# Optimization experiments

Hardware: AMD Instinct MI355X
Metric: run time of the kernel (lower is better)

Reference implementation:

```python
import jax, jax.numpy as jnp
import numpy as np

V, NJ, NB, NP, NK = 6890, 24, 10, 207, 19
PARENTS = [-1,0,0,0,1,2,3,4,5,6,7,8,9,9,9,12,13,14,16,17,18,19,20,21]


def setup_inputs() -> dict:
    key = jax.random.key(0)
    ks = jax.random.split(key, 9)
    N = 2048
    return {
        "beta": jax.random.normal(ks[0], (N, NB), jnp.float32),
        "theta": jax.random.normal(ks[1], (N, NJ, 3), jnp.float32) * 0.2,
        "trans": jax.random.normal(ks[2], (N, 3), jnp.float32),
        "shapedirs": jax.random.normal(ks[3], (V, 3, NB), jnp.float32) * 0.03,
        "v_template": jax.random.normal(ks[4], (V, 3), jnp.float32),
        "J_regressor": jax.random.uniform(ks[5], (NJ, V), jnp.float32) / V,
        "posedirs": jax.random.normal(ks[6], (V, 3, NP), jnp.float32) * 0.01,
        "weights": jax.nn.softmax(jax.random.normal(ks[7], (V, NJ), jnp.float32) * 4.0, axis=-1),
        "joint_regressor": jax.random.uniform(ks[8], (V, NK), jnp.float32) / V,
    }


def rodrigues(r):
    # r: [M,3] axis-angle -> [M,3,3] rotation matrices
    theta = jnp.maximum(jnp.linalg.norm(r, axis=-1, keepdims=True),
                        jnp.finfo(r.dtype).tiny)  # [M,1]
    rh = r / theta
    c = jnp.cos(theta)[:, :, None]  # [M,1,1]
    s = jnp.sin(theta)[:, :, None]
    z = jnp.zeros_like(rh[:, 0])
    K = jnp.stack([z, -rh[:, 2], rh[:, 1],
                   rh[:, 2], z, -rh[:, 0],
                   -rh[:, 1], rh[:, 0], z], axis=1).reshape(-1, 3, 3)
    outer = rh[:, :, None] * rh[:, None, :]
    return c * jnp.eye(3, dtype=r.dtype) + (1.0 - c) * outer + s * K


def reference(beta, theta, trans, shapedirs, v_template, J_regressor, posedirs, weights, joint_regressor):
    N = beta.shape[0]
    dt = beta.dtype
    v_shaped = jnp.einsum('nb,vcb->nvc', beta, shapedirs) + v_template  # [N,V,3]
    J = jnp.einsum('jv,nvc->njc', J_regressor, v_shaped)                # [N,24,3]
    # pose rotations and pose blendshapes
    R = rodrigues(theta.reshape(-1, 3)).reshape(N, NJ, 3, 3)
    lrotmin = (R[:, 1:] - jnp.eye(3, dtype=dt)).reshape(N, NP)
    v_posed = v_shaped + jnp.einsum('np,vcp->nvc', lrotmin, posedirs)
    # kinematic chain: 24 small 4x4 transforms with parent dependencies
    bottom = jnp.broadcast_to(jnp.array([0., 0., 0., 1.], dtype=dt), (N, 1, 4))
    def make_A(Ri, t):  # [N,3,3],[N,3] -> [N,4,4]
        return jnp.concatenate([jnp.concatenate([Ri, t[:, :, None]], axis=2), bottom], axis=1)
    G = [make_A(R[:, 0], J[:, 0])]
    for i in range(1, NJ):
        p = PARENTS[i]
        G.append(G[p] @ make_A(R[:, i], J[:, i] - J[:, p]))
    G = jnp.stack(G, axis=1)  # [N,24,4,4]
    # subtract rest-pose joint contribution
    Jh = jnp.concatenate([J, jnp.zeros((N, NJ, 1), dt)], axis=2)[..., None]  # [N,24,4,1]
    corr = G @ Jh
    G_rel = G - jnp.concatenate([jnp.zeros((N, NJ, 4, 3), dt), corr], axis=3)
    # linear blend skinning
    T = jnp.einsum('njab,vj->nvab', G_rel, weights)  # [N,V,4,4]
    vh = jnp.concatenate([v_posed, jnp.ones((N, V, 1), dt)], axis=2)  # [N,V,4]
    v = jnp.einsum('nvab,nvb->nva', T, vh)[..., :3]
    verts = v + trans[:, None, :]
    joints = jnp.einsum('nvc,vk->nkc', verts, joint_regressor)  # [N,19,3]
    return verts, joints
```

## Files before the change

kernel.cpp:

```cpp
#include <hip/hip_runtime.h>

#define V      6890
#define NJ     24
#define NB     10
#define NP     207
#define NK     19
#define NBATCH 2048
#define KP     224
#define KC     217
#define VC     (V*3)
#define VCP    20736
#define BN     64
#define BV     64
#define VST4   260
#define VSEG   1723
#define JSP    18
#define JCH    9
#define BWSZ   1536

using bh8   = __attribute__((ext_vector_type(8))) short;
using u16x4 = __attribute__((ext_vector_type(4))) unsigned short;
using u16x8 = __attribute__((ext_vector_type(8))) unsigned short;
using f32x4 = __attribute__((ext_vector_type(4))) float;

__constant__ int PAR[NJ] = {-1,0,0,0,1,2,3,4,5,6,7,8,9,9,9,12,13,14,16,17,18,19,20,21};

__device__ __forceinline__ unsigned short f2bf(float f) {
    unsigned int u = __float_as_uint(f);
    u += 0x7FFFu + ((u >> 16) & 1u);
    return (unsigned short)(u >> 16);
}
__device__ __forceinline__ float bf2f(unsigned short h) {
    return __uint_as_float((unsigned int)h << 16);
}

__global__ __launch_bounds__(256) void k_prep(const float* __restrict__ Jreg,
                                              const float* __restrict__ vtmpl,
                                              const float* __restrict__ sdirs,
                                              const float* __restrict__ pdirs,
                                              const float* __restrict__ jreg,
                                              float* __restrict__ JB,
                                              unsigned short* __restrict__ Bmat,
                                              unsigned short* __restrict__ JbigT) {
    int blk = blockIdx.x, tid = threadIdx.x;
    if (blk < 792) {
        int vs = blk & 3, og = blk >> 2;
        int o = og*4 + (tid >> 6);
        int lane = tid & 63;
        int j = o/33, t = o%33, c = t/11, m = t%11;
        int lo = vs*VSEG + lane, hi = min(V, vs*VSEG + VSEG);
        const float* jr = Jreg + j*V;
        float s = 0.f;
        if (m == 0) { for (int v = lo; v < hi; v += 64) s += jr[v] * vtmpl[v*3 + c]; }
        else        { for (int v = lo; v < hi; v += 64) s += jr[v] * sdirs[(v*3 + c)*NB + (m-1)]; }
        #pragma unroll
        for (int d = 1; d < 64; d <<= 1) s += __shfl_xor(s, d);
        if (lane == 0) atomicAdd(&JB[(j*3 + c)*11 + m], s);
    } else if (blk < 792 + 2268) {
        int gid = (blk - 792)*256 + tid;
        int vc = gid / 28, q = gid - vc*28;
        int k0 = q*8;
        unsigned short out[8];
        if (vc >= VC) {
            #pragma unroll
            for (int j = 0; j < 8; ++j) out[j] = 0;
        } else if (q >= 2 && q <= 26) {
            const float* p = pdirs + (size_t)vc*NP + (k0 - NB);
            #pragma unroll
            for (int j = 0; j < 8; ++j) out[j] = f2bf(p[j]);
        } else {
            #pragma unroll
            for (int j = 0; j < 8; ++j) {
                int k = k0 + j;
                float val;
                if (k < NB)       val = sdirs[vc*NB + k];
                else if (k < KC)  val = pdirs[(size_t)vc*NP + (k - NB)];
                else if (k == KC) val = vtmpl[vc];
                else              val = 0.f;
                out[j] = f2bf(val);
            }
        }
        *(u16x8*)&Bmat[((size_t)(k0 >> 5)*VCP + vc)*32 + (k0 & 31)] = *(u16x8*)out;
    } else {
        int gid = (blk - 792 - 2268)*256 + tid;
        int kc = gid / (VCP/8), u = gid - kc*(VCP/8);
        int vc0 = u*8;
        unsigned short out[8];
        #pragma unroll
        for (int j = 0; j < 8; ++j) out[j] = 0;
        if (kc < NK*3) {
            #pragma unroll
            for (int j = 0; j < 8; ++j) {
                int vc = vc0 + j;
                if (vc < VC && (vc % 3) == (kc % 3))
                    out[j] = f2bf(jreg[(vc/3)*NK + (kc/3)]);
            }
        }
        *(u16x8*)&JbigT[((size_t)(vc0 >> 5)*64 + kc)*32 + (vc0 & 31)] = *(u16x8*)out;
    }
}

__global__ __launch_bounds__(64) void k_pern(const float* __restrict__ beta,
                                             const float* __restrict__ theta,
                                             const float* __restrict__ trans,
                                             const float* __restrict__ JB,
                                             unsigned short* __restrict__ Arow,
                                             unsigned short* __restrict__ Gt) {
    int n = blockIdx.x, tid = threadIdx.x;
    __shared__ float Rsm[NJ][9];
    __shared__ float Jsm[NJ][3];
    __shared__ float Gsm[NJ][12];

    if (tid < NJ) {
        const float* th = theta + (n*NJ + tid)*3;
        float x = th[0], y = th[1], z = th[2];
        float nrm = sqrtf(x*x + y*y + z*z);
        float t = fmaxf(nrm, 1.1754944e-38f);
        float inv = 1.0f / t;
        float rx = x*inv, ry = y*inv, rz = z*inv;
        float c = cosf(t), s = sinf(t), oc = 1.0f - c;
        Rsm[tid][0] = c + oc*rx*rx;      Rsm[tid][1] = oc*rx*ry - s*rz;  Rsm[tid][2] = oc*rx*rz + s*ry;
        Rsm[tid][3] = oc*ry*rx + s*rz;   Rsm[tid][4] = c + oc*ry*ry;     Rsm[tid][5] = oc*ry*rz - s*rx;
        Rsm[tid][6] = oc*rz*rx - s*ry;   Rsm[tid][7] = oc*rz*ry + s*rx;  Rsm[tid][8] = c + oc*rz*rz;
    } else if (tid < 2*NJ) {
        int j = tid - NJ;
        #pragma unroll
        for (int c = 0; c < 3; ++c) {
            float s = JB[(j*3+c)*11 + 0];
            #pragma unroll
            for (int b = 0; b < NB; ++b) s += JB[(j*3+c)*11 + 1 + b] * beta[n*NB + b];
            Jsm[j][c] = s;
        }
    }
    __syncthreads();

    if (tid < 12) {
        int a = tid >> 2, b = tid & 3;
        Gsm[0][a*4+b] = (b < 3) ? Rsm[0][a*3+b] : Jsm[0][a];
    }
    __syncthreads();
    for (int i = 1; i < NJ; ++i) {
        if (tid < 12) {
            int a = tid >> 2, b = tid & 3;
            int p = PAR[i];
            float acc = (b == 3) ? Gsm[p][a*4+3] : 0.0f;
            #pragma unroll
            for (int k = 0; k < 3; ++k) {
                float aval = (b < 3) ? Rsm[i][k*3+b] : (Jsm[i][k] - Jsm[p][k]);
                acc += Gsm[p][a*4+k] * aval;
            }
            Gsm[i][a*4+b] = acc;
        }
        __syncthreads();
    }
    if (tid < NJ) {
        int j = tid;
        #pragma unroll
        for (int a = 0; a < 3; ++a) {
            float t3 = Gsm[j][a*4+3]
                     - (Gsm[j][a*4+0]*Jsm[j][0] + Gsm[j][a*4+1]*Jsm[j][1] + Gsm[j][a*4+2]*Jsm[j][2])
                     + trans[n*3 + a];
            Gsm[j][a*4+3] = t3;
        }
    }
    __syncthreads();
    unsigned short* gt = Gt + n*512;
    for (int idx = tid; idx < 512; idx += 64) {
        int e = idx >> 5, j = idx & 31;
        float val = (e < 12 && j < NJ) ? Gsm[j][e] : 0.0f;
        gt[idx] = f2bf(val);
    }
    for (int k = tid; k < KP; k += 64) {
        float val;
        if (k < NB) val = beta[n*NB + k];
        else if (k < KC) {
            int p = k - NB; int jj = p/9 + 1; int rr = p%9;
            val = Rsm[jj][rr] - ((rr==0 || rr==4 || rr==8) ? 1.0f : 0.0f);
        } else if (k == KC) val = 1.0f;
        else val = 0.0f;
        Arow[((size_t)(k >> 5)*NBATCH + n)*32 + (k & 31)] = f2bf(val);
    }
}

__global__ __launch_bounds__(512) void k_main(const unsigned short* __restrict__ Arow,
                                              const unsigned short* __restrict__ Bmat,
                                              const unsigned short* __restrict__ Gt,
                                              const float* __restrict__ weights,
                                              float* __restrict__ verts) {
    __shared__ __attribute__((aligned(16))) char smem[49152];
    unsigned short* Bw   = (unsigned short*)smem;
    unsigned short* vhsm = (unsigned short*)smem;

    int tid = threadIdx.x;
    int wv = tid >> 6, lane = tid & 63;
    int l15 = lane & 15, jg = lane >> 4;
    int wn = wv >> 2, wc = wv & 3;
    int nb = blockIdx.x, vb = blockIdx.y;
    int n0 = nb * BN, v0 = vb * BV, vc0 = v0 * 3;

    int c4[3];
    #pragma unroll
    for (int ct = 0; ct < 3; ++ct) {
        int vcw = wc*48 + ct*16 + l15;
        c4[ct] = (vcw/3)*4 + vcw%3;
    }
    int tri = (((lane % 3)*16) + lane/3) * 4;

    unsigned short* bw0 = &Bw[wv*2*BWSZ];
    unsigned short* bw1 = bw0 + BWSZ;
    const unsigned short* bsrc0 = Bmat + ((size_t)(vc0 + wc*48))*32;
    auto stageB = [&](unsigned short* dst, int ks) {
        const unsigned short* s = bsrc0 + (size_t)ks*VCP*32;
        #pragma unroll
        for (int i = 0; i < 3; ++i) {
            __builtin_amdgcn_global_load_lds(
                (const __attribute__((address_space(1))) void*)(s + i*512 + (size_t)lane*8),
                (__attribute__((address_space(3))) void*)(dst + i*512),
                16, 0, 0);
        }
    };

    const unsigned short* abase = Arow + ((size_t)(n0 + wn*32) + l15)*32 + jg*8;

    stageB(bw0, 0);
    bh8 aA0 = *(const bh8*)(abase);
    bh8 aA1 = *(const bh8*)(abase + 16*32);
    __builtin_amdgcn_sched_barrier(0);
    stageB(bw1, 1);
    bh8 aB0 = *(const bh8*)(abase + (size_t)NBATCH*32);
    bh8 aB1 = *(const bh8*)(abase + (size_t)NBATCH*32 + 16*32);
    __builtin_amdgcn_sched_barrier(0);

    f32x4 acc[2][3] = {};
    #pragma unroll
    for (int ks = 0; ks < 7; ++ks) {
        if (ks < 6) asm volatile("s_waitcnt vmcnt(5)" ::: "memory");
        else        asm volatile("s_waitcnt vmcnt(0)" ::: "memory");
        __builtin_amdgcn_sched_barrier(0);
        unsigned short* bcur = (ks & 1) ? bw1 : bw0;
        bh8 b0 = *(const bh8*)(bcur + ( 0 + l15)*32 + jg*8);
        bh8 b1 = *(const bh8*)(bcur + (16 + l15)*32 + jg*8);
        bh8 b2 = *(const bh8*)(bcur + (32 + l15)*32 + jg*8);
        asm volatile("s_waitcnt lgkmcnt(0)" ::: "memory");
        __builtin_amdgcn_sched_barrier(0);
        bh8 a0 = (ks & 1) ? aB0 : aA0;
        bh8 a1 = (ks & 1) ? aB1 : aA1;
        if (ks + 2 <= 6) {
            stageB(bcur, ks + 2);
            if (ks & 1) {
                aB0 = *(const bh8*)(abase + (size_t)(ks+2)*NBATCH*32);
                aB1 = *(const bh8*)(abase + (size_t)(ks+2)*NBATCH*32 + 16*32);
            } else {
                aA0 = *(const bh8*)(abase + (size_t)(ks+2)*NBATCH*32);
                aA1 = *(const bh8*)(abase + (size_t)(ks+2)*NBATCH*32 + 16*32);
            }
            __builtin_amdgcn_sched_barrier(0);
        }
        acc[0][0] = __builtin_amdgcn_mfma_f32_16x16x32_bf16(a0, b0, acc[0][0], 0, 0, 0);
        acc[0][1] = __builtin_amdgcn_mfma_f32_16x16x32_bf16(a0, b1, acc[0][1], 0, 0, 0);
        acc[0][2] = __builtin_amdgcn_mfma_f32_16x16x32_bf16(a0, b2, acc[0][2], 0, 0, 0);
        acc[1][0] = __builtin_amdgcn_mfma_f32_16x16x32_bf16(a1, b0, acc[1][0], 0, 0, 0);
        acc[1][1] = __builtin_amdgcn_mfma_f32_16x16x32_bf16(a1, b1, acc[1][1], 0, 0, 0);
        acc[1][2] = __builtin_amdgcn_mfma_f32_16x16x32_bf16(a1, b2, acc[1][2], 0, 0, 0);
    }

    __syncthreads();

    #pragma unroll
    for (int mt = 0; mt < 2; ++mt)
        #pragma unroll
        for (int ct = 0; ct < 3; ++ct)
            #pragma unroll
            for (int r = 0; r < 4; ++r)
                vhsm[(wn*32 + mt*16 + jg*4 + r)*VST4 + c4[ct]] = f2bf(acc[mt][ct][r]);
    __syncthreads();

    bh8 wfrag[4];
    #pragma unroll
    for (int mt = 0; mt < 4; ++mt) {
        int vr = v0 + mt*16 + l15;
        bh8 f = {0,0,0,0,0,0,0,0};
        if (jg < 3 && vr < V) {
            const float4* wp = (const float4*)(weights + (size_t)vr*NJ + jg*8);
            float4 w0 = wp[0], w1 = wp[1];
            f[0]=(short)f2bf(w0.x); f[1]=(short)f2bf(w0.y); f[2]=(short)f2bf(w0.z); f[3]=(short)f2bf(w0.w);
            f[4]=(short)f2bf(w1.x); f[5]=(short)f2bf(w1.y); f[6]=(short)f2bf(w1.z); f[7]=(short)f2bf(w1.w);
        }
        wfrag[mt] = f;
    }

    const unsigned short* gbase = Gt + ((size_t)(n0 + wv*8))*512 + l15*32 + jg*8;
    bh8 gcur = *(const bh8*)gbase;
    #pragma unroll
    for (int nl = 0; nl < 8; ++nl) {
        bh8 gnxt = gcur;
        if (nl < 7) gnxt = *(const bh8*)(gbase + (nl+1)*512);
        int n_loc = wv*8 + nl;
        #pragma unroll
        for (int mt = 0; mt < 4; ++mt) {
            f32x4 z = {0.f, 0.f, 0.f, 0.f};
            f32x4 t = __builtin_amdgcn_mfma_f32_16x16x32_bf16(gcur, wfrag[mt], z, 0, 0, 0);
            u16x4 vh4 = *(const u16x4*)&vhsm[n_loc*VST4 + (mt*16 + l15)*4];
            float p = t[0]*bf2f(vh4[0]) + t[1]*bf2f(vh4[1]) + t[2]*bf2f(vh4[2]) + t[3];
            float pp = __int_as_float(__builtin_amdgcn_ds_bpermute(tri, __float_as_int(p)));
            int col = vc0 + mt*48 + lane;
            if (lane < 48 && col < VC)
                verts[(size_t)(n0 + n_loc)*VC + col] = pp;
        }
        gcur = gnxt;
    }
}

__global__ __launch_bounds__(256) void k_joints(const float* __restrict__ verts,
                                                const unsigned short* __restrict__ JbigT,
                                                float* __restrict__ jpart) {
    __shared__ __attribute__((aligned(16))) unsigned short vt[32*128];

    int tid = threadIdx.x;
    int lane = tid & 63, wv = tid >> 6;
    int l15 = lane & 15, jg = lane >> 4;
    int nt = blockIdx.x, ks = blockIdx.y;
    int n0 = nt * 32;
    int step0 = ks * (JCH*4);

    int row[4], c4[4];
    #pragma unroll
    for (int i = 0; i < 4; ++i) {
        int idx = i*256 + tid;
        row[i] = idx >> 5; c4[i] = idx & 31;
    }

    float2 rg[8];
    auto issue = [&](int ch) {
        int k0f = (step0 + ch*4) * 32;
        #pragma unroll
        for (int i = 0; i < 4; ++i) {
            const float* p = verts + (size_t)(n0 + row[i])*VC + k0f + c4[i]*4;
            rg[2*i+0] = *(const float2*)(p);
            rg[2*i+1] = *(const float2*)(p+2);
        }
    };

    issue(0);
    f32x4 acc[2] = {};
    #pragma unroll 1
    for (int ch = 0; ch < JCH; ++ch) {
        __syncthreads();
        #pragma unroll
        for (int i = 0; i < 4; ++i) {
            u16x4 w;
            w[0] = f2bf(rg[2*i].x); w[1] = f2bf(rg[2*i].y);
            w[2] = f2bf(rg[2*i+1].x); w[3] = f2bf(rg[2*i+1].y);
            int sidx = (row[i]*128 + c4[i]*4) ^ ((row[i] & 7) << 3);
            *(u16x4*)&vt[sidx] = w;
        }
        __syncthreads();
        if (ch + 1 < JCH) issue(ch + 1);
        #pragma unroll
        for (int kk = 0; kk < 4; ++kk) {
            int r0 = l15, r1 = 16 + l15;
            bh8 a0 = *(const bh8*)&vt[(r0*128 + kk*32 + jg*8) ^ ((r0 & 7) << 3)];
            bh8 a1 = *(const bh8*)&vt[(r1*128 + kk*32 + jg*8) ^ ((r1 & 7) << 3)];
            bh8 b  = *(const bh8*)(JbigT + ((size_t)(step0 + ch*4 + kk)*64 + wv*16 + l15)*32 + jg*8);
            acc[0] = __builtin_amdgcn_mfma_f32_16x16x32_bf16(a0, b, acc[0], 0, 0, 0);
            acc[1] = __builtin_amdgcn_mfma_f32_16x16x32_bf16(a1, b, acc[1], 0, 0, 0);
        }
    }
    float* jp = jpart + ((size_t)ks*NBATCH + n0)*64 + wv*16 + l15;
    #pragma unroll
    for (int mt = 0; mt < 2; ++mt)
        #pragma unroll
        for (int r = 0; r < 4; ++r)
            jp[(size_t)(mt*16 + jg*4 + r)*64] = acc[mt][r];
}

__global__ __launch_bounds__(256) void k_jred(const float* __restrict__ jpart,
                                              float* __restrict__ joints) {
    int idx = blockIdx.x*256 + threadIdx.x;
    if (idx >= NBATCH*NK*3) return;
    int n = idx / (NK*3), i = idx - n*(NK*3);
    float s = 0.f;
    #pragma unroll
    for (int ks = 0; ks < JSP; ++ks)
        s += jpart[((size_t)ks*NBATCH + n)*64 + i];
    joints[idx] = s;
}

extern "C" void kernel_launch(void* const* d_in, const int* in_sizes, int n_in,
                              void* d_out, int out_size, void* d_ws, size_t ws_size,
                              hipStream_t stream) {
    const float* beta  = (const float*)d_in[0];
    const float* theta = (const float*)d_in[1];
    const float* trans = (const float*)d_in[2];
    const float* sdirs = (const float*)d_in[3];
    const float* vtmpl = (const float*)d_in[4];
    const float* jregJ = (const float*)d_in[5];
    const float* pdirs = (const float*)d_in[6];
    const float* wgts  = (const float*)d_in[7];
    const float* jregK = (const float*)d_in[8];

    float* verts  = (float*)d_out;
    float* joints = verts + (size_t)NBATCH * VC;

    char* ws = (char*)d_ws;
    float*          JB    = (float*)ws;
    unsigned short* Arow  = (unsigned short*)(ws + 4096);
    unsigned short* Gt    = (unsigned short*)(ws + 4096 + 917504);
    unsigned short* Bmat  = (unsigned short*)(ws + 4096 + 917504 + 2097152);
    unsigned short* JbigT = (unsigned short*)(ws + 4096 + 917504 + 2097152 + 9289728);
    float*          jpart = (float*)(ws + 4096 + 917504 + 2097152 + 9289728 + 2654208);

    hipMemsetAsync(JB, 0, 4096, stream);

    k_prep <<<792 + 2268 + 648, 256, 0, stream>>>(jregJ, vtmpl, sdirs, pdirs, jregK, JB, Bmat, JbigT);
    k_pern <<<NBATCH, 64, 0, stream>>>(beta, theta, trans, JB, Arow, Gt);
    dim3 g4(NBATCH/BN, (V + BV - 1)/BV);
    k_main <<<g4, 512, 0, stream>>>(Arow, Bmat, Gt, wgts, verts);
    dim3 g5(NBATCH/32, JSP);
    k_joints<<<g5, 256, 0, stream>>>(verts, JbigT, jpart);
    k_jred <<<(NBATCH*NK*3 + 255)/256, 256, 0, stream>>>(jpart, joints);
}
```

Measured before the change: 150.3 us.

## Double vertex tile per block so each wave covers all 64 batch rows

Widens the k_main vertex tile from 64 to 128 vertices per block. Each of the 8 waves now owns a distinct 48-column slice and computes all 64 batch rows, instead of splitting 32 rows by 4 column groups. Each staged B slice is reused across four A tiles rather than two, and the grid holds half as many blocks. In exchange, accumulator and A-fragment register use grows, LDS rises to about 66KB, which may cut occupancy, and the skinning loop does twice the MFMA work per wave.

Result: slower. 153.8 us (+2.3%).

```diff
diff --git a/kernel.cpp b/kernel.cpp
--- a/kernel.cpp
+++ b/kernel.cpp
@@ -11,8 +11,9 @@
 #define VC     (V*3)
 #define VCP    20736
 #define BN     64
-#define BV     64
-#define VST4   260
+#define BV     128
+#define BVC    384
+#define VST4   516
 #define VSEG   1723
 #define JSP    18
 #define JCH    9
@@ -187,28 +188,27 @@
                                               const unsigned short* __restrict__ Gt,
                                               const float* __restrict__ weights,
                                               float* __restrict__ verts) {
-    __shared__ __attribute__((aligned(16))) char smem[49152];
+    __shared__ __attribute__((aligned(16))) char smem[66048];
     unsigned short* Bw   = (unsigned short*)smem;
     unsigned short* vhsm = (unsigned short*)smem;
 
     int tid = threadIdx.x;
     int wv = tid >> 6, lane = tid & 63;
     int l15 = lane & 15, jg = lane >> 4;
-    int wn = wv >> 2, wc = wv & 3;
     int nb = blockIdx.x, vb = blockIdx.y;
     int n0 = nb * BN, v0 = vb * BV, vc0 = v0 * 3;
 
     int c4[3];
     #pragma unroll
     for (int ct = 0; ct < 3; ++ct) {
-        int vcw = wc*48 + ct*16 + l15;
+        int vcw = wv*48 + ct*16 + l15;
         c4[ct] = (vcw/3)*4 + vcw%3;
     }
     int tri = (((lane % 3)*16) + lane/3) * 4;
 
     unsigned short* bw0 = &Bw[wv*2*BWSZ];
     unsigned short* bw1 = bw0 + BWSZ;
-    const unsigned short* bsrc0 = Bmat + ((size_t)(vc0 + wc*48))*32;
+    const unsigned short* bsrc0 = Bmat + ((size_t)(vc0 + wv*48))*32;
     auto stageB = [&](unsigned short* dst, int ks) {
         const unsigned short* s = bsrc0 + (size_t)ks*VCP*32;
         #pragma unroll
@@ -220,21 +220,25 @@
         }
     };
 
-    const unsigned short* abase = Arow + ((size_t)(n0 + wn*32) + l15)*32 + jg*8;
-
+    const unsigned short* abase = Arow + ((size_t)n0 + l15)*32 + jg*8;
+    auto loadA = [&](bh8* a, int ks) {
+        #pragma unroll
+        for (int mt = 0; mt < 4; ++mt)
+            a[mt] = *(const bh8*)(abase + (size_t)ks*NBATCH*32 + mt*16*32);
+    };
+
+    bh8 aA[4], aB[4];
     stageB(bw0, 0);
-    bh8 aA0 = *(const bh8*)(abase);
-    bh8 aA1 = *(const bh8*)(abase + 16*32);
+    loadA(aA, 0);
     __builtin_amdgcn_sched_barrier(0);
     stageB(bw1, 1);
-    bh8 aB0 = *(const bh8*)(abase + (size_t)NBATCH*32);
-    bh8 aB1 = *(const bh8*)(abase + (size_t)NBATCH*32 + 16*32);
+    loadA(aB, 1);
     __builtin_amdgcn_sched_barrier(0);
 
-    f32x4 acc[2][3] = {};
+    f32x4 acc[4][3] = {};
     #pragma unroll
     for (int ks = 0; ks < 7; ++ks) {
-        if (ks < 6) asm volatile("s_waitcnt vmcnt(5)" ::: "memory");
+        if (ks < 6) asm volatile("s_waitcnt vmcnt(7)" ::: "memory");
         else        asm volatile("s_waitcnt vmcnt(0)" ::: "memory");
         __builtin_amdgcn_sched_barrier(0);
         unsigned short* bcur = (ks & 1) ? bw1 : bw0;
@@ -243,17 +247,14 @@
         bh8 b2 = *(const bh8*)(bcur + (32 + l15)*32 + jg*8);
         asm volatile("s_waitcnt lgkmcnt(0)" ::: "memory");
         __builtin_amdgcn_sched_barrier(0);
-        bh8 a0 = (ks & 1) ? aB0 : aA0;
-        bh8 a1 = (ks & 1) ? aB1 : aA1;
+        bh8 a0 = (ks & 1) ? aB[0] : aA[0];
+        bh8 a1 = (ks & 1) ? aB[1] : aA[1];
+        bh8 a2 = (ks & 1) ? aB[2] : aA[2];
+        bh8 a3 = (ks & 1) ? aB[3] : aA[3];
         if (ks + 2 <= 6) {
             stageB(bcur, ks + 2);
-            if (ks & 1) {
-                aB0 = *(const bh8*)(abase + (size_t)(ks+2)*NBATCH*32);
-                aB1 = *(const bh8*)(abase + (size_t)(ks+2)*NBATCH*32 + 16*32);
-            } else {
-                aA0 = *(const bh8*)(abase + (size_t)(ks+2)*NBATCH*32);
-                aA1 = *(const bh8*)(abase + (size_t)(ks+2)*NBATCH*32 + 16*32);
-            }
+            if (ks & 1) loadA(aB, ks + 2);
+            else        loadA(aA, ks + 2);
             __builtin_amdgcn_sched_barrier(0);
         }
         acc[0][0] = __builtin_amdgcn_mfma_f32_16x16x32_bf16(a0, b0, acc[0][0], 0, 0, 0);
@@ -262,22 +263,28 @@
         acc[1][0] = __builtin_amdgcn_mfma_f32_16x16x32_bf16(a1, b0, acc[1][0], 0, 0, 0);
         acc[1][1] = __builtin_amdgcn_mfma_f32_16x16x32_bf16(a1, b1, acc[1][1], 0, 0, 0);
         acc[1][2] = __builtin_amdgcn_mfma_f32_16x16x32_bf16(a1, b2, acc[1][2], 0, 0, 0);
+        acc[2][0] = __builtin_amdgcn_mfma_f32_16x16x32_bf16(a2, b0, acc[2][0], 0, 0, 0);
+        acc[2][1] = __builtin_amdgcn_mfma_f32_16x16x32_bf16(a2, b1, acc[2][1], 0, 0, 0);
+        acc[2][2] = __builtin_amdgcn_mfma_f32_16x16x32_bf16(a2, b2, acc[2][2], 0, 0, 0);
+        acc[3][0] = __builtin_amdgcn_mfma_f32_16x16x32_bf16(a3, b0, acc[3][0], 0, 0, 0);
+        acc[3][1] = __builtin_amdgcn_mfma_f32_16x16x32_bf16(a3, b1, acc[3][1], 0, 0, 0);
+        acc[3][2] = __builtin_amdgcn_mfma_f32_16x16x32_bf16(a3, b2, acc[3][2], 0, 0, 0);
     }
 
     __syncthreads();
 
     #pragma unroll
-    for (int mt = 0; mt < 2; ++mt)
+    for (int mt = 0; mt < 4; ++mt)
         #pragma unroll
         for (int ct = 0; ct < 3; ++ct)
             #pragma unroll
             for (int r = 0; r < 4; ++r)
-                vhsm[(wn*32 + mt*16 + jg*4 + r)*VST4 + c4[ct]] = f2bf(acc[mt][ct][r]);
+                vhsm[(mt*16 + jg*4 + r)*VST4 + c4[ct]] = f2bf(acc[mt][ct][r]);
     __syncthreads();
 
-    bh8 wfrag[4];
-    #pragma unroll
-    for (int mt = 0; mt < 4; ++mt) {
+    bh8 wfrag[8];
+    #pragma unroll
+    for (int mt = 0; mt < 8; ++mt) {
         int vr = v0 + mt*16 + l15;
         bh8 f = {0,0,0,0,0,0,0,0};
         if (jg < 3 && vr < V) {
@@ -297,7 +304,7 @@
         if (nl < 7) gnxt = *(const bh8*)(gbase + (nl+1)*512);
         int n_loc = wv*8 + nl;
         #pragma unroll
-        for (int mt = 0; mt < 4; ++mt) {
+        for (int mt = 0; mt < 8; ++mt) {
             f32x4 z = {0.f, 0.f, 0.f, 0.f};
             f32x4 t = __builtin_amdgcn_mfma_f32_16x16x32_bf16(gcur, wfrag[mt], z, 0, 0, 0);
             u16x4 vh4 = *(const u16x4*)&vhsm[n_loc*VST4 + (mt*16 + l15)*4];
@@ -414,7 +421,7 @@
 
     k_prep <<<792 + 2268 + 648, 256, 0, stream>>>(jregJ, vtmpl, sdirs, pdirs, jregK, JB, Bmat, JbigT);
     k_pern <<<NBATCH, 64, 0, stream>>>(beta, theta, trans, JB, Arow, Gt);
-    dim3 g4(NBATCH/BN, (V + BV - 1)/BV);
+    dim3 g4(NBATCH/BN, VCP/BVC);
     k_main <<<g4, 512, 0, stream>>>(Arow, Bmat, Gt, wgts, verts);
     dim3 g5(NBATCH/32, JSP);
     k_joints<<<g5, 256, 0, stream>>>(verts, JbigT, jpart);
```
